# Kernel optimization log

Hardware: AMD Instinct MI355X
Metric: run time of the kernel (lower is better)

## Reference

```python
import jax, jax.numpy as jnp
import numpy as np

N, E = 20000, 320000
IN_F, EF, H, C = 2, 1, 128, 2
BN_S = 1.0 / float(np.sqrt(1.0 + 1e-5))  # eval-mode BatchNorm1d with running mean 0, var 1


def _gated_gcn_conv(h, e, src, dst, p, act, residual):
    # DGL GatedGCNConv: e' = C e + D h_src + E h_dst;
    # h' = A h + sum_{in-edges} sigmoid(e') * B h_src / (sum sigmoid(e') + 1e-6)
    Aw, Ab, Bw, Bb, Cw, Cb, Dw, Db, Ew, Eb, bhg, bhb, beg, beb = p
    h_in, e_in = h, e
    Ah = h @ Aw + Ab
    Bh = h @ Bw + Bb
    Dh = h @ Dw + Db
    Eh = h @ Ew + Eb
    e2 = e @ Cw + Cb + Dh[src] + Eh[dst]          # [E, H]
    sig = jax.nn.sigmoid(e2)
    num = jax.ops.segment_sum(sig * Bh[src], dst, num_segments=N)  # [N, H]
    den = jax.ops.segment_sum(sig, dst, num_segments=N)            # [N, H]
    h2 = Ah + num / (den + 1e-6)
    # BatchNorm (eval): (x - 0)/sqrt(1 + eps) * gamma + beta
    h2 = bhg * (h2 * BN_S) + bhb
    e2 = beg * (e2 * BN_S) + beb
    h2, e2 = act(h2), act(e2)
    if residual:
        h2 = h2 + h_in
        e2 = e2 + e_in
    return h2, e2


def _forward(node_feats, edge_feats, src, dst, P):
    (a0_w, a0_b, b0_w, b0_b, c0_w, c0_b, d0_w, d0_b, e0_w, e0_b,
     bnh0_g, bnh0_b, bne0_g, bne0_b,
     aL_w, aL_b, bL_w, bL_b, cL_w, cL_b, dL_w, dL_b, eL_w, eL_b,
     bnhL_g, bnhL_b, bneL_g, bneL_b,
     mlp_w1, mlp_b1, mlp_w2, mlp_b2) = P
    h, e = node_feats, edge_feats
    # layer 0: elu inside conv, residual off (2->128, 1->128)
    p0 = (a0_w, a0_b, b0_w, b0_b, c0_w, c0_b, d0_w, d0_b, e0_w, e0_b,
          bnh0_g, bnh0_b, bne0_g, bne0_b)
    h, e = _gated_gcn_conv(h, e, src, dst, p0, jax.nn.elu, residual=False)
    h = jax.nn.leaky_relu(h)
    e = jax.nn.leaky_relu(e)
    # layers 1..2: leaky_relu inside conv, residual on (128->128)
    for l in range(2):
        pl = (aL_w[l], aL_b[l], bL_w[l], bL_b[l], cL_w[l], cL_b[l],
              dL_w[l], dL_b[l], eL_w[l], eL_b[l],
              bnhL_g[l], bnhL_b[l], bneL_g[l], bneL_b[l])
        h, e = _gated_gcn_conv(h, e, src, dst, pl, jax.nn.leaky_relu, residual=True)
        h = jax.nn.leaky_relu(h)
        e = jax.nn.leaky_relu(e)
    # edge classifier: gather endpoints, concat with edge feats, MLP
    edge_repr = jnp.concatenate([h[src], h[dst], e], axis=1)  # [E, 3H]
    hid = jax.nn.relu(edge_repr @ mlp_w1 + mlp_b1)
    return hid @ mlp_w2 + mlp_b2                               # [E, C]


PARAM_NAMES = ["a0_w", "a0_b", "b0_w", "b0_b", "c0_w", "c0_b", "d0_w", "d0_b",
               "e0_w", "e0_b", "bnh0_g", "bnh0_b", "bne0_g", "bne0_b",
               "aL_w", "aL_b", "bL_w", "bL_b", "cL_w", "cL_b", "dL_w", "dL_b",
               "eL_w", "eL_b", "bnhL_g", "bnhL_b", "bneL_g", "bneL_b",
               "mlp_w1", "mlp_b1", "mlp_w2", "mlp_b2"]


def setup_inputs() -> dict:
    key = jax.random.key(0)
    ks = iter(jax.random.split(key, 64))
    nrm = lambda shp: jax.random.normal(next(ks), shp, dtype=jnp.float32) * 0.05
    inp = {}
    inp["node_feats"] = jax.random.normal(next(ks), (N, IN_F), dtype=jnp.float32)
    inp["edge_feats"] = jax.random.normal(next(ks), (E, EF), dtype=jnp.float32)
    inp["src"] = jax.random.randint(next(ks), (E,), 0, N, dtype=jnp.int32)
    inp["dst"] = jax.random.randint(next(ks), (E,), 0, N, dtype=jnp.int32)
    # layer 0 linears (A,B,D,E: in->H; C: edge->H), biases zero-init like common practice
    for nm, din in [("a0", IN_F), ("b0", IN_F), ("c0", EF), ("d0", IN_F), ("e0", IN_F)]:
        inp[nm + "_w"] = nrm((din, H))
        inp[nm + "_b"] = nrm((H,))
    inp["bnh0_g"] = jnp.ones((H,), jnp.float32)
    inp["bnh0_b"] = jnp.zeros((H,), jnp.float32)
    inp["bne0_g"] = jnp.ones((H,), jnp.float32)
    inp["bne0_b"] = jnp.zeros((H,), jnp.float32)
    # layers 1..2 stacked
    for nm in ["aL", "bL", "cL", "dL", "eL"]:
        inp[nm + "_w"] = nrm((2, H, H))
        inp[nm + "_b"] = nrm((2, H))
    inp["bnhL_g"] = jnp.ones((2, H), jnp.float32)
    inp["bnhL_b"] = jnp.zeros((2, H), jnp.float32)
    inp["bneL_g"] = jnp.ones((2, H), jnp.float32)
    inp["bneL_b"] = jnp.zeros((2, H), jnp.float32)
    # edge MLP
    inp["mlp_w1"] = nrm((3 * H, H))
    inp["mlp_b1"] = nrm((H,))
    inp["mlp_w2"] = nrm((H, C))
    inp["mlp_b2"] = nrm((C,))
    return inp


def reference(node_feats, edge_feats, src, dst,
              a0_w, a0_b, b0_w, b0_b, c0_w, c0_b, d0_w, d0_b, e0_w, e0_b,
              bnh0_g, bnh0_b, bne0_g, bne0_b,
              aL_w, aL_b, bL_w, bL_b, cL_w, cL_b, dL_w, dL_b, eL_w, eL_b,
              bnhL_g, bnhL_b, bneL_g, bneL_b,
              mlp_w1, mlp_b1, mlp_w2, mlp_b2):
    P = (a0_w, a0_b, b0_w, b0_b, c0_w, c0_b, d0_w, d0_b, e0_w, e0_b,
         bnh0_g, bnh0_b, bne0_g, bne0_b,
         aL_w, aL_b, bL_w, bL_b, cL_w, cL_b, dL_w, dL_b, eL_w, eL_b,
         bnhL_g, bnhL_b, bneL_g, bneL_b,
         mlp_w1, mlp_b1, mlp_w2, mlp_b2)
    return _forward(node_feats, edge_feats, src, dst, P)
```

## Files before the change

### kernel.cpp

```cpp
#include <hip/hip_runtime.h>
#include <hip/hip_bf16.h>
#include <math.h>

#define NN 20000
#define NE 320000
#define H 128
#define NH (NN * H)

typedef short bf16x8 __attribute__((ext_vector_type(8)));
typedef float f32x4 __attribute__((ext_vector_type(4)));
typedef unsigned short u16x8 __attribute__((ext_vector_type(8)));

__device__ __forceinline__ float lrelu(float x) { return x > 0.f ? x : 0.01f * x; }
__device__ __forceinline__ float eluf(float x)  { return x > 0.f ? x : expm1f(x); }
__device__ __forceinline__ float sigf(float x)  { return 1.f / (1.f + __expf(-x)); }
__device__ __forceinline__ unsigned short f2b(float x) {
    __hip_bfloat16 h = __float2bfloat16(x);
    return *reinterpret_cast<unsigned short*>(&h);
}
__device__ __forceinline__ float b2f(unsigned short u) {
    __hip_bfloat16 h = *reinterpret_cast<__hip_bfloat16*>(&u);
    return __bfloat162float(h);
}
#define BN_S 0.99999500003749973f

struct PackPtrs { const float* w[13]; };
__global__ __launch_bounds__(256) void k_pack(PackPtrs p, unsigned short* __restrict__ dst) {
    int gid = blockIdx.x * 256 + threadIdx.x;
    int m = gid >> 11;
    int r = gid & 2047;
    int t = r >> 8, kk = (r >> 6) & 3, lane = r & 63;
    const float* W = p.w[m];
    int col = t * 16 + (lane & 15);
    int krow = kk * 32 + (lane >> 4) * 8;
    unsigned short* o = dst + (size_t)m * 16384 + (size_t)r * 8;
#pragma unroll
    for (int j = 0; j < 8; ++j) o[j] = f2b(W[(krow + j) * H + col]);
}

__global__ __launch_bounds__(256) void k_deg(const int* __restrict__ dst, int* __restrict__ deg) {
    int e = blockIdx.x * 256 + threadIdx.x;
    if (e < NE) atomicAdd(&deg[dst[e]], 1);
}

__global__ __launch_bounds__(256) void k_scan(const int* __restrict__ deg,
                                              int* __restrict__ off, int* __restrict__ cursor) {
    __shared__ int sums[256];
    const int t = threadIdx.x;
    const int per = (NN + 255) / 256;
    const int base = t * per;
    int s = 0;
    for (int i = 0; i < per; ++i) { int idx = base + i; if (idx < NN) s += deg[idx]; }
    sums[t] = s;
    __syncthreads();
    for (int d = 1; d < 256; d <<= 1) {
        int v = (t >= d) ? sums[t - d] : 0;
        __syncthreads();
        sums[t] += v;
        __syncthreads();
    }
    int run = (t == 0) ? 0 : sums[t - 1];
    for (int i = 0; i < per; ++i) {
        int idx = base + i;
        if (idx < NN) { off[idx] = run; cursor[idx] = run; run += deg[idx]; }
    }
}

__global__ __launch_bounds__(256) void k_fill(const int* __restrict__ dst,
                                              int* __restrict__ cursor, int* __restrict__ csr) {
    int e = blockIdx.x * 256 + threadIdx.x;
    if (e < NE) {
        int pos = atomicAdd(&cursor[dst[e]], 1);
        csr[pos] = e;
    }
}

__global__ __launch_bounds__(256) void k_seqs(const int* __restrict__ csr,
                                              const int* __restrict__ src,
                                              const int* __restrict__ dst,
                                              int* __restrict__ srcseq,
                                              int* __restrict__ dstseq) {
    int pos = blockIdx.x * 256 + threadIdx.x;
    if (pos < NE) {
        int eid = csr[pos];
        srcseq[pos] = src[eid];
        dstseq[pos] = dst[eid];
    }
}

__global__ __launch_bounds__(256) void k_nodelin0(
        const float* __restrict__ nf,
        const float* __restrict__ wa, const float* __restrict__ ba,
        const float* __restrict__ wb, const float* __restrict__ bb,
        const float* __restrict__ wd, const float* __restrict__ bd,
        const float* __restrict__ we, const float* __restrict__ be,
        float* __restrict__ lin) {
    int idx = blockIdx.x * 256 + threadIdx.x;
    int n = idx >> 7, c = idx & 127;
    float x0 = nf[n * 2], x1 = nf[n * 2 + 1];
    lin[0 * NH + idx] = fmaf(x0, wa[c], fmaf(x1, wa[128 + c], ba[c]));
    lin[1 * NH + idx] = fmaf(x0, wb[c], fmaf(x1, wb[128 + c], bb[c]));
    lin[2 * NH + idx] = fmaf(x0, wd[c], fmaf(x1, wd[128 + c], bd[c]));
    lin[3 * NH + idx] = fmaf(x0, we[c], fmaf(x1, we[128 + c], be[c]));
}

__global__ __launch_bounds__(256) void k_edge0(
        const float* __restrict__ ef,
        const float* __restrict__ cw, const float* __restrict__ cb,
        const int* __restrict__ src, const int* __restrict__ dst,
        const float* __restrict__ lin,
        const float* __restrict__ g, const float* __restrict__ bt,
        unsigned short* __restrict__ ebuf) {
    const int tid = threadIdx.x;
    const int e  = blockIdx.x * 8 + (tid >> 5);
    const int c0 = (tid & 31) * 4;
    const int s = src[e], d = dst[e];
    const float ev = ef[e];
    const float4 cw4 = *(const float4*)(cw + c0);
    const float4 cb4 = *(const float4*)(cb + c0);
    const float4 Dh  = *(const float4*)(lin + 2 * NH + (size_t)s * H + c0);
    const float4 Eh  = *(const float4*)(lin + 3 * NH + (size_t)d * H + c0);
    const float4 g4  = *(const float4*)(g + c0);
    const float4 bt4 = *(const float4*)(bt + c0);
    float e2[4] = { fmaf(ev, cw4.x, cb4.x) + Dh.x + Eh.x,
                    fmaf(ev, cw4.y, cb4.y) + Dh.y + Eh.y,
                    fmaf(ev, cw4.z, cb4.z) + Dh.z + Eh.z,
                    fmaf(ev, cw4.w, cb4.w) + Dh.w + Eh.w };
    const float gg[4] = { g4.x, g4.y, g4.z, g4.w };
    const float bb[4] = { bt4.x, bt4.y, bt4.z, bt4.w };
    ushort4 u;
    u.x = f2b(lrelu(eluf(fmaf(gg[0], e2[0] * BN_S, bb[0]))));
    u.y = f2b(lrelu(eluf(fmaf(gg[1], e2[1] * BN_S, bb[1]))));
    u.z = f2b(lrelu(eluf(fmaf(gg[2], e2[2] * BN_S, bb[2]))));
    u.w = f2b(lrelu(eluf(fmaf(gg[3], e2[3] * BN_S, bb[3]))));
    *(ushort4*)(ebuf + (size_t)e * H + c0) = u;
}

__global__ __launch_bounds__(256) void k_agg0(
        const int* __restrict__ off, const int* __restrict__ deg,
        const int* __restrict__ csr, const int* __restrict__ srcseq,
        const float* __restrict__ ef, const float* __restrict__ cw, const float* __restrict__ cb,
        const float* __restrict__ lin,
        const float* __restrict__ g, const float* __restrict__ bt,
        float* __restrict__ hout) {
    const int tid = threadIdx.x;
    const int n = blockIdx.x * 2 + (tid >> 7);
    const int c = tid & 127;
    const int base = off[n], dg = deg[n];
    float num = 0.f, den = 0.f;
    const float Ehn = lin[3 * NH + (size_t)n * H + c];
    const float cwc = cw[c], cbc = cb[c];
    int i = 0;
    for (; i + 2 <= dg; i += 2) {
        int ea = csr[base + i], eb = csr[base + i + 1];
        int sa = srcseq[base + i], sb = srcseq[base + i + 1];
        float xa = fmaf(ef[ea], cwc, cbc) + lin[2 * NH + (size_t)sa * H + c] + Ehn;
        float xb = fmaf(ef[eb], cwc, cbc) + lin[2 * NH + (size_t)sb * H + c] + Ehn;
        float ga = sigf(xa), gb = sigf(xb);
        num = fmaf(ga, lin[1 * NH + (size_t)sa * H + c], num); den += ga;
        num = fmaf(gb, lin[1 * NH + (size_t)sb * H + c], num); den += gb;
    }
    if (i < dg) {
        int ea = csr[base + i];
        int sa = srcseq[base + i];
        float xa = fmaf(ef[ea], cwc, cbc) + lin[2 * NH + (size_t)sa * H + c] + Ehn;
        float ga = sigf(xa);
        num = fmaf(ga, lin[1 * NH + (size_t)sa * H + c], num); den += ga;
    }
    float h2 = lin[(size_t)n * H + c] + num / (den + 1e-6f);
    h2 = fmaf(g[c], h2 * BN_S, bt[c]);
    h2 = eluf(h2);
    hout[(size_t)n * H + c] = lrelu(h2);
}

__global__ __launch_bounds__(256) void k_agg(
        const int* __restrict__ off, const int* __restrict__ deg,
        const int* __restrict__ srcseq,
        const unsigned short* __restrict__ e2seq,
        const float* __restrict__ lin,
        const float* __restrict__ g, const float* __restrict__ bt,
        const float* __restrict__ hin, float* __restrict__ hout) {
    const int tid = threadIdx.x;
    const int n = blockIdx.x * 2 + (tid >> 7);
    const int c = tid & 127;
    const int base = off[n], dg = deg[n];
    float num = 0.f, den = 0.f;
    int i = 0;
    for (; i + 2 <= dg; i += 2) {
        int sa = srcseq[base + i], sb = srcseq[base + i + 1];
        float xa = b2f(e2seq[(size_t)(base + i) * H + c]);
        float xb = b2f(e2seq[(size_t)(base + i + 1) * H + c]);
        float ga = sigf(xa), gb = sigf(xb);
        num = fmaf(ga, lin[1 * NH + (size_t)sa * H + c], num); den += ga;
        num = fmaf(gb, lin[1 * NH + (size_t)sb * H + c], num); den += gb;
    }
    if (i < dg) {
        int sa = srcseq[base + i];
        float xa = b2f(e2seq[(size_t)(base + i) * H + c]);
        float ga = sigf(xa);
        num = fmaf(ga, lin[1 * NH + (size_t)sa * H + c], num); den += ga;
    }
    float h2 = lin[(size_t)n * H + c] + num / (den + 1e-6f);
    h2 = fmaf(g[c], h2 * BN_S, bt[c]);
    h2 = lrelu(h2);
    h2 += hin[(size_t)n * H + c];
    hout[(size_t)n * H + c] = lrelu(h2);
}

__global__ __launch_bounds__(256) void k_nodegemm(
        const float* __restrict__ h,
        const unsigned short* __restrict__ wpack,
        const float* __restrict__ ba, const float* __restrict__ bb,
        const float* __restrict__ bd, const float* __restrict__ be,
        float* __restrict__ lin) {
    __shared__ __align__(16) unsigned short AT[64][136];
    const int tid = threadIdx.x;
    const int nbase = blockIdx.x * 64;
    const int which = blockIdx.y;
    const unsigned short* Wp = wpack + (size_t)which * 16384;
    const float* B = which == 0 ? ba : which == 1 ? bb : which == 2 ? bd : be;
#pragma unroll
    for (int rep = 0; rep < 8; ++rep) {
        int flat = (rep * 256 + tid) * 4;
        int r = flat >> 7, k0 = flat & 127;
        int n = nbase + r;
        float4 v = make_float4(0.f, 0.f, 0.f, 0.f);
        if (n < NN) v = *(const float4*)(h + (size_t)n * H + k0);
        ushort4 u = { f2b(v.x), f2b(v.y), f2b(v.z), f2b(v.w) };
        *(ushort4*)(&AT[r][k0]) = u;
    }
    __syncthreads();
    const int lane = tid & 63, wave = tid >> 6;
    const int lrow = lane & 15, quad = lane >> 4;
    f32x4 acc[8] = {};
#pragma unroll
    for (int kk = 0; kk < 4; ++kk) {
        bf16x8 af = *(const bf16x8*)(&AT[wave * 16 + lrow][kk * 32 + quad * 8]);
#pragma unroll
        for (int t = 0; t < 8; ++t) {
            bf16x8 bfv = *(const bf16x8*)(Wp + ((t * 4 + kk) * 64 + lane) * 8);
            acc[t] = __builtin_amdgcn_mfma_f32_16x16x32_bf16(af, bfv, acc[t], 0, 0, 0);
        }
    }
#pragma unroll
    for (int t = 0; t < 8; ++t) {
        int col = t * 16 + lrow;
        float bv = B[col];
#pragma unroll
        for (int reg = 0; reg < 4; ++reg) {
            int n = nbase + wave * 16 + quad * 4 + reg;
            if (n < NN)
                lin[(size_t)which * NH + (size_t)n * H + col] = acc[t][reg] + bv;
        }
    }
}

__global__ __launch_bounds__(256) void k_edgegemm(
        unsigned short* __restrict__ ebuf,
        unsigned short* __restrict__ e2seq,
        const unsigned short* __restrict__ Wp,
        const float* __restrict__ cb,
        const int* __restrict__ csr,
        const int* __restrict__ srcseq, const int* __restrict__ dstseq,
        const float* __restrict__ lin,
        const float* __restrict__ g, const float* __restrict__ bt) {
    __shared__ __align__(16) unsigned short AT[64][136];
    const int tid = threadIdx.x;
    const int ebase = blockIdx.x * 64;
#pragma unroll
    for (int rep = 0; rep < 4; ++rep) {
        int flat = (rep * 256 + tid) * 8;
        int r = flat >> 7, k0 = flat & 127;
        int eid = csr[ebase + r];
        *(u16x8*)(&AT[r][k0]) = *(const u16x8*)(ebuf + (size_t)eid * H + k0);
    }
    __syncthreads();
    const int lane = tid & 63, wave = tid >> 6;
    const int lrow = lane & 15, quad = lane >> 4;
    f32x4 acc[8] = {};
#pragma unroll
    for (int kk = 0; kk < 4; ++kk) {
        bf16x8 af = *(const bf16x8*)(&AT[wave * 16 + lrow][kk * 32 + quad * 8]);
#pragma unroll
        for (int t = 0; t < 8; ++t) {
            bf16x8 bfv = *(const bf16x8*)(Wp + ((t * 4 + kk) * 64 + lane) * 8);
            acc[t] = __builtin_amdgcn_mfma_f32_16x16x32_bf16(af, bfv, acc[t], 0, 0, 0);
        }
    }
    const int r0 = ebase + wave * 16 + quad * 4;
    const int rr0 = wave * 16 + quad * 4;
    int eid[4], sv[4], dv[4];
#pragma unroll
    for (int reg = 0; reg < 4; ++reg) {
        eid[reg] = csr[r0 + reg];
        sv[reg]  = srcseq[r0 + reg];
        dv[reg]  = dstseq[r0 + reg];
    }
#pragma unroll
    for (int t = 0; t < 8; ++t) {
        int col = t * 16 + lrow;
        float cbv = cb[col], gv = g[col], btv = bt[col];
#pragma unroll
        for (int reg = 0; reg < 4; ++reg) {
            float Dh = lin[2 * NH + (size_t)sv[reg] * H + col];
            float Eh = lin[3 * NH + (size_t)dv[reg] * H + col];
            float e2 = acc[t][reg] + cbv + Dh + Eh;
            e2seq[(size_t)(r0 + reg) * H + col] = f2b(e2);
            float tt = lrelu(fmaf(gv, e2 * BN_S, btv));
            float ein = b2f(AT[rr0 + reg][col]);
            ebuf[(size_t)eid[reg] * H + col] = f2b(lrelu(tt + ein));
        }
    }
}

__global__ __launch_bounds__(256) void k_mlp(
        const float* __restrict__ h, const unsigned short* __restrict__ ebuf,
        const int* __restrict__ src, const int* __restrict__ dst,
        const unsigned short* __restrict__ w1p,
        const float* __restrict__ b1,
        const float* __restrict__ w2, const float* __restrict__ b2,
        float* __restrict__ out) {
    __shared__ __align__(16) unsigned short AT[64][136];
    const int tid = threadIdx.x;
    const int ebase = blockIdx.x * 64;
    const int lane = tid & 63, wave = tid >> 6;
    const int lrow = lane & 15, quad = lane >> 4;
    f32x4 acc[8] = {};
    for (int chunk = 0; chunk < 3; ++chunk) {
        if (chunk < 2) {
            const int* idx = chunk == 0 ? src : dst;
#pragma unroll
            for (int rep = 0; rep < 8; ++rep) {
                int flat = (rep * 256 + tid) * 4;
                int r = flat >> 7, k0 = flat & 127;
                int e = ebase + r;
                float4 v = *(const float4*)(h + (size_t)idx[e] * H + k0);
                ushort4 u = { f2b(v.x), f2b(v.y), f2b(v.z), f2b(v.w) };
                *(ushort4*)(&AT[r][k0]) = u;
            }
        } else {
#pragma unroll
            for (int rep = 0; rep < 4; ++rep) {
                int flat = (rep * 256 + tid) * 8;
                int r = flat >> 7, k0 = flat & 127;
                int e = ebase + r;
                *(u16x8*)(&AT[r][k0]) = *(const u16x8*)(ebuf + (size_t)e * H + k0);
            }
        }
        __syncthreads();
        const unsigned short* Wp = w1p + (size_t)chunk * 16384;
#pragma unroll
        for (int kk = 0; kk < 4; ++kk) {
            bf16x8 af = *(const bf16x8*)(&AT[wave * 16 + lrow][kk * 32 + quad * 8]);
#pragma unroll
            for (int t = 0; t < 8; ++t) {
                bf16x8 bfv = *(const bf16x8*)(Wp + ((t * 4 + kk) * 64 + lane) * 8);
                acc[t] = __builtin_amdgcn_mfma_f32_16x16x32_bf16(af, bfv, acc[t], 0, 0, 0);
            }
        }
        __syncthreads();
    }
    const float b20 = b2[0], b21 = b2[1];
#pragma unroll
    for (int reg = 0; reg < 4; ++reg) {
        float p0 = 0.f, p1 = 0.f;
#pragma unroll
        for (int t = 0; t < 8; ++t) {
            int col = t * 16 + lrow;
            float hv = fmaxf(acc[t][reg] + b1[col], 0.f);
            p0 = fmaf(hv, w2[col * 2], p0);
            p1 = fmaf(hv, w2[col * 2 + 1], p1);
        }
#pragma unroll
        for (int off = 8; off; off >>= 1) {
            p0 += __shfl_xor(p0, off, 16);
            p1 += __shfl_xor(p1, off, 16);
        }
        if (lrow == 0) {
            int e = ebase + wave * 16 + quad * 4 + reg;
            out[e * 2]     = p0 + b20;
            out[e * 2 + 1] = p1 + b21;
        }
    }
}

extern "C" void kernel_launch(void* const* d_in, const int* in_sizes, int n_in,
                              void* d_out, int out_size, void* d_ws, size_t ws_size,
                              hipStream_t stream) {
    const float* nf  = (const float*)d_in[0];
    const float* ef  = (const float*)d_in[1];
    const int*   src = (const int*)d_in[2];
    const int*   dst = (const int*)d_in[3];
    const float *a0w = (const float*)d_in[4],  *a0b = (const float*)d_in[5];
    const float *b0w = (const float*)d_in[6],  *b0b = (const float*)d_in[7];
    const float *c0w = (const float*)d_in[8],  *c0b = (const float*)d_in[9];
    const float *d0w = (const float*)d_in[10], *d0b = (const float*)d_in[11];
    const float *e0w = (const float*)d_in[12], *e0b = (const float*)d_in[13];
    const float *bnh0g = (const float*)d_in[14], *bnh0b = (const float*)d_in[15];
    const float *bne0g = (const float*)d_in[16], *bne0b = (const float*)d_in[17];
    const float *aLw = (const float*)d_in[18], *aLb = (const float*)d_in[19];
    const float *bLw = (const float*)d_in[20], *bLb = (const float*)d_in[21];
    const float *cLw = (const float*)d_in[22], *cLb = (const float*)d_in[23];
    const float *dLw = (const float*)d_in[24], *dLb = (const float*)d_in[25];
    const float *eLw = (const float*)d_in[26], *eLb = (const float*)d_in[27];
    const float *bnhLg = (const float*)d_in[28], *bnhLb = (const float*)d_in[29];
    const float *bneLg = (const float*)d_in[30], *bneLb = (const float*)d_in[31];
    const float *w1 = (const float*)d_in[32], *b1 = (const float*)d_in[33];
    const float *w2 = (const float*)d_in[34], *b2 = (const float*)d_in[35];
    float* out = (float*)d_out;

    char* ws = (char*)d_ws;
    unsigned short* ebuf  = (unsigned short*)ws;
    unsigned short* e2seq = ebuf + (size_t)NE * H;
    float* lin = (float*)(e2seq + (size_t)NE * H);
    float* h0  = lin + 4ull * NH;
    float* h1  = h0 + NH;
    int* deg    = (int*)(h1 + NH);
    int* off    = deg + NN;
    int* cursor = off + NN;
    int* csr    = cursor + NN;
    int* srcseq = csr + NE;
    int* dstseq = srcseq + NE;
    unsigned short* wpack = (unsigned short*)(dstseq + NE);

    PackPtrs pp;
    const size_t HH = (size_t)H * H;
    for (int l = 0; l < 2; ++l) {
        pp.w[l * 5 + 0] = aLw + l * HH;
        pp.w[l * 5 + 1] = bLw + l * HH;
        pp.w[l * 5 + 2] = dLw + l * HH;
        pp.w[l * 5 + 3] = eLw + l * HH;
        pp.w[l * 5 + 4] = cLw + l * HH;
    }
    pp.w[10] = w1; pp.w[11] = w1 + HH; pp.w[12] = w1 + 2 * HH;
    k_pack<<<104, 256, 0, stream>>>(pp, wpack);

    hipMemsetAsync(deg, 0, NN * sizeof(int), stream);
    k_deg<<<(NE + 255) / 256, 256, 0, stream>>>(dst, deg);
    k_scan<<<1, 256, 0, stream>>>(deg, off, cursor);
    k_fill<<<(NE + 255) / 256, 256, 0, stream>>>(dst, cursor, csr);
    k_seqs<<<(NE + 255) / 256, 256, 0, stream>>>(csr, src, dst, srcseq, dstseq);

    k_nodelin0<<<NN * H / 256, 256, 0, stream>>>(nf, a0w, a0b, b0w, b0b, d0w, d0b, e0w, e0b, lin);
    k_edge0<<<NE / 8, 256, 0, stream>>>(ef, c0w, c0b, src, dst, lin, bne0g, bne0b, ebuf);
    k_agg0<<<NN / 2, 256, 0, stream>>>(off, deg, csr, srcseq, ef, c0w, c0b,
                                       lin, bnh0g, bnh0b, h0);

    for (int l = 0; l < 2; ++l) {
        const float* hin = (l == 0) ? h0 : h1;
        float* hout      = (l == 0) ? h1 : h0;
        k_nodegemm<<<dim3(313, 4), 256, 0, stream>>>(hin,
            wpack + (size_t)l * 5 * 16384,
            aLb + l * H, bLb + l * H, dLb + l * H, eLb + l * H, lin);
        k_edgegemm<<<NE / 64, 256, 0, stream>>>(ebuf, e2seq,
                                                wpack + (size_t)(l * 5 + 4) * 16384,
                                                cLb + l * H, csr, srcseq, dstseq, lin,
                                                bneLg + l * H, bneLb + l * H);
        k_agg<<<NN / 2, 256, 0, stream>>>(off, deg, srcseq, e2seq,
                                          lin, bnhLg + l * H, bnhLb + l * H,
                                          hin, hout);
    }

    k_mlp<<<NE / 64, 256, 0, stream>>>(h0, ebuf, src, dst, wpack + 10ull * 16384,
                                       b1, w2, b2, out);

    (void)in_sizes; (void)n_in; (void)out_size; (void)ws_size;
}
```

Measured before the change: 764.1 us.

## Precompute node-side MLP projections per node and keep bf16 node feature copies

```diff
diff --git a/kernel.cpp b/kernel.cpp
--- a/kernel.cpp
+++ b/kernel.cpp
@@ -142,7 +142,7 @@
         const float* __restrict__ ef, const float* __restrict__ cw, const float* __restrict__ cb,
         const float* __restrict__ lin,
         const float* __restrict__ g, const float* __restrict__ bt,
-        float* __restrict__ hout) {
+        float* __restrict__ hout, unsigned short* __restrict__ hbout) {
     const int tid = threadIdx.x;
     const int n = blockIdx.x * 2 + (tid >> 7);
     const int c = tid & 127;
@@ -151,16 +151,22 @@
     const float Ehn = lin[3 * NH + (size_t)n * H + c];
     const float cwc = cw[c], cbc = cb[c];
     int i = 0;
-    for (; i + 2 <= dg; i += 2) {
-        int ea = csr[base + i], eb = csr[base + i + 1];
-        int sa = srcseq[base + i], sb = srcseq[base + i + 1];
-        float xa = fmaf(ef[ea], cwc, cbc) + lin[2 * NH + (size_t)sa * H + c] + Ehn;
-        float xb = fmaf(ef[eb], cwc, cbc) + lin[2 * NH + (size_t)sb * H + c] + Ehn;
-        float ga = sigf(xa), gb = sigf(xb);
-        num = fmaf(ga, lin[1 * NH + (size_t)sa * H + c], num); den += ga;
-        num = fmaf(gb, lin[1 * NH + (size_t)sb * H + c], num); den += gb;
-    }
-    if (i < dg) {
+    for (; i + 4 <= dg; i += 4) {
+        int e0 = csr[base + i],     e1 = csr[base + i + 1];
+        int e2_ = csr[base + i + 2], e3 = csr[base + i + 3];
+        int s0 = srcseq[base + i],     s1 = srcseq[base + i + 1];
+        int s2 = srcseq[base + i + 2], s3 = srcseq[base + i + 3];
+        float x0 = fmaf(ef[e0], cwc, cbc) + lin[2 * NH + (size_t)s0 * H + c] + Ehn;
+        float x1 = fmaf(ef[e1], cwc, cbc) + lin[2 * NH + (size_t)s1 * H + c] + Ehn;
+        float x2 = fmaf(ef[e2_], cwc, cbc) + lin[2 * NH + (size_t)s2 * H + c] + Ehn;
+        float x3 = fmaf(ef[e3], cwc, cbc) + lin[2 * NH + (size_t)s3 * H + c] + Ehn;
+        float g0 = sigf(x0), g1 = sigf(x1), g2 = sigf(x2), g3 = sigf(x3);
+        num = fmaf(g0, lin[1 * NH + (size_t)s0 * H + c], num); den += g0;
+        num = fmaf(g1, lin[1 * NH + (size_t)s1 * H + c], num); den += g1;
+        num = fmaf(g2, lin[1 * NH + (size_t)s2 * H + c], num); den += g2;
+        num = fmaf(g3, lin[1 * NH + (size_t)s3 * H + c], num); den += g3;
+    }
+    for (; i < dg; ++i) {
         int ea = csr[base + i];
         int sa = srcseq[base + i];
         float xa = fmaf(ef[ea], cwc, cbc) + lin[2 * NH + (size_t)sa * H + c] + Ehn;
@@ -170,7 +176,9 @@
     float h2 = lin[(size_t)n * H + c] + num / (den + 1e-6f);
     h2 = fmaf(g[c], h2 * BN_S, bt[c]);
     h2 = eluf(h2);
-    hout[(size_t)n * H + c] = lrelu(h2);
+    float r = lrelu(h2);
+    hout[(size_t)n * H + c] = r;
+    hbout[(size_t)n * H + c] = f2b(r);
 }
 
 __global__ __launch_bounds__(256) void k_agg(
@@ -179,22 +187,28 @@
         const unsigned short* __restrict__ e2seq,
         const float* __restrict__ lin,
         const float* __restrict__ g, const float* __restrict__ bt,
-        const float* __restrict__ hin, float* __restrict__ hout) {
+        const float* __restrict__ hin, float* __restrict__ hout,
+        unsigned short* __restrict__ hbout) {
     const int tid = threadIdx.x;
     const int n = blockIdx.x * 2 + (tid >> 7);
     const int c = tid & 127;
     const int base = off[n], dg = deg[n];
     float num = 0.f, den = 0.f;
     int i = 0;
-    for (; i + 2 <= dg; i += 2) {
-        int sa = srcseq[base + i], sb = srcseq[base + i + 1];
-        float xa = b2f(e2seq[(size_t)(base + i) * H + c]);
-        float xb = b2f(e2seq[(size_t)(base + i + 1) * H + c]);
-        float ga = sigf(xa), gb = sigf(xb);
-        num = fmaf(ga, lin[1 * NH + (size_t)sa * H + c], num); den += ga;
-        num = fmaf(gb, lin[1 * NH + (size_t)sb * H + c], num); den += gb;
-    }
-    if (i < dg) {
+    for (; i + 4 <= dg; i += 4) {
+        int s0 = srcseq[base + i],     s1 = srcseq[base + i + 1];
+        int s2 = srcseq[base + i + 2], s3 = srcseq[base + i + 3];
+        float x0 = b2f(e2seq[(size_t)(base + i) * H + c]);
+        float x1 = b2f(e2seq[(size_t)(base + i + 1) * H + c]);
+        float x2 = b2f(e2seq[(size_t)(base + i + 2) * H + c]);
+        float x3 = b2f(e2seq[(size_t)(base + i + 3) * H + c]);
+        float g0 = sigf(x0), g1 = sigf(x1), g2 = sigf(x2), g3 = sigf(x3);
+        num = fmaf(g0, lin[1 * NH + (size_t)s0 * H + c], num); den += g0;
+        num = fmaf(g1, lin[1 * NH + (size_t)s1 * H + c], num); den += g1;
+        num = fmaf(g2, lin[1 * NH + (size_t)s2 * H + c], num); den += g2;
+        num = fmaf(g3, lin[1 * NH + (size_t)s3 * H + c], num); den += g3;
+    }
+    for (; i < dg; ++i) {
         int sa = srcseq[base + i];
         float xa = b2f(e2seq[(size_t)(base + i) * H + c]);
         float ga = sigf(xa);
@@ -204,11 +218,13 @@
     h2 = fmaf(g[c], h2 * BN_S, bt[c]);
     h2 = lrelu(h2);
     h2 += hin[(size_t)n * H + c];
-    hout[(size_t)n * H + c] = lrelu(h2);
+    float r = lrelu(h2);
+    hout[(size_t)n * H + c] = r;
+    hbout[(size_t)n * H + c] = f2b(r);
 }
 
 __global__ __launch_bounds__(256) void k_nodegemm(
-        const float* __restrict__ h,
+        const unsigned short* __restrict__ hb,
         const unsigned short* __restrict__ wpack,
         const float* __restrict__ ba, const float* __restrict__ bb,
         const float* __restrict__ bd, const float* __restrict__ be,
@@ -220,14 +236,13 @@
     const unsigned short* Wp = wpack + (size_t)which * 16384;
     const float* B = which == 0 ? ba : which == 1 ? bb : which == 2 ? bd : be;
 #pragma unroll
-    for (int rep = 0; rep < 8; ++rep) {
-        int flat = (rep * 256 + tid) * 4;
+    for (int rep = 0; rep < 4; ++rep) {
+        int flat = (rep * 256 + tid) * 8;
         int r = flat >> 7, k0 = flat & 127;
         int n = nbase + r;
-        float4 v = make_float4(0.f, 0.f, 0.f, 0.f);
-        if (n < NN) v = *(const float4*)(h + (size_t)n * H + k0);
-        ushort4 u = { f2b(v.x), f2b(v.y), f2b(v.z), f2b(v.w) };
-        *(ushort4*)(&AT[r][k0]) = u;
+        u16x8 v = {};
+        if (n < NN) v = *(const u16x8*)(hb + (size_t)n * H + k0);
+        *(u16x8*)(&AT[r][k0]) = v;
     }
     __syncthreads();
     const int lane = tid & 63, wave = tid >> 6;
@@ -251,6 +266,51 @@
             int n = nbase + wave * 16 + quad * 4 + reg;
             if (n < NN)
                 lin[(size_t)which * NH + (size_t)n * H + col] = acc[t][reg] + bv;
+        }
+    }
+}
+
+__global__ __launch_bounds__(256) void k_pgemm(
+        const unsigned short* __restrict__ hb,
+        const unsigned short* __restrict__ w1p,
+        const float* __restrict__ b1,
+        float* __restrict__ P) {
+    __shared__ __align__(16) unsigned short AT[64][136];
+    const int tid = threadIdx.x;
+    const int nbase = blockIdx.x * 64;
+    const int y = blockIdx.y;
+    const unsigned short* Wp = w1p + (size_t)y * 16384;
+#pragma unroll
+    for (int rep = 0; rep < 4; ++rep) {
+        int flat = (rep * 256 + tid) * 8;
+        int r = flat >> 7, k0 = flat & 127;
+        int n = nbase + r;
+        u16x8 v = {};
+        if (n < NN) v = *(const u16x8*)(hb + (size_t)n * H + k0);
+        *(u16x8*)(&AT[r][k0]) = v;
+    }
+    __syncthreads();
+    const int lane = tid & 63, wave = tid >> 6;
+    const int lrow = lane & 15, quad = lane >> 4;
+    f32x4 acc[8] = {};
+#pragma unroll
+    for (int kk = 0; kk < 4; ++kk) {
+        bf16x8 af = *(const bf16x8*)(&AT[wave * 16 + lrow][kk * 32 + quad * 8]);
+#pragma unroll
+        for (int t = 0; t < 8; ++t) {
+            bf16x8 bfv = *(const bf16x8*)(Wp + ((t * 4 + kk) * 64 + lane) * 8);
+            acc[t] = __builtin_amdgcn_mfma_f32_16x16x32_bf16(af, bfv, acc[t], 0, 0, 0);
+        }
+    }
+#pragma unroll
+    for (int t = 0; t < 8; ++t) {
+        int col = t * 16 + lrow;
+        float bv = (y == 0) ? b1[col] : 0.f;
+#pragma unroll
+        for (int reg = 0; reg < 4; ++reg) {
+            int n = nbase + wave * 16 + quad * 4 + reg;
+            if (n < NN)
+                P[(size_t)y * NH + (size_t)n * H + col] = acc[t][reg] + bv;
         }
     }
 }
@@ -313,61 +373,53 @@
     }
 }
 
-__global__ __launch_bounds__(256) void k_mlp(
-        const float* __restrict__ h, const unsigned short* __restrict__ ebuf,
+__global__ __launch_bounds__(256) void k_mlp2(
+        const unsigned short* __restrict__ ebuf,
+        const float* __restrict__ P,
         const int* __restrict__ src, const int* __restrict__ dst,
-        const unsigned short* __restrict__ w1p,
-        const float* __restrict__ b1,
+        const unsigned short* __restrict__ w1p2,
         const float* __restrict__ w2, const float* __restrict__ b2,
         float* __restrict__ out) {
     __shared__ __align__(16) unsigned short AT[64][136];
     const int tid = threadIdx.x;
     const int ebase = blockIdx.x * 64;
+#pragma unroll
+    for (int rep = 0; rep < 4; ++rep) {
+        int flat = (rep * 256 + tid) * 8;
+        int r = flat >> 7, k0 = flat & 127;
+        *(u16x8*)(&AT[r][k0]) = *(const u16x8*)(ebuf + (size_t)(ebase + r) * H + k0);
+    }
+    __syncthreads();
     const int lane = tid & 63, wave = tid >> 6;
     const int lrow = lane & 15, quad = lane >> 4;
     f32x4 acc[8] = {};
-    for (int chunk = 0; chunk < 3; ++chunk) {
-        if (chunk < 2) {
-            const int* idx = chunk == 0 ? src : dst;
-#pragma unroll
-            for (int rep = 0; rep < 8; ++rep) {
-                int flat = (rep * 256 + tid) * 4;
-                int r = flat >> 7, k0 = flat & 127;
-                int e = ebase + r;
-                float4 v = *(const float4*)(h + (size_t)idx[e] * H + k0);
-                ushort4 u = { f2b(v.x), f2b(v.y), f2b(v.z), f2b(v.w) };
-                *(ushort4*)(&AT[r][k0]) = u;
-            }
-        } else {
-#pragma unroll
-            for (int rep = 0; rep < 4; ++rep) {
-                int flat = (rep * 256 + tid) * 8;
-                int r = flat >> 7, k0 = flat & 127;
-                int e = ebase + r;
-                *(u16x8*)(&AT[r][k0]) = *(const u16x8*)(ebuf + (size_t)e * H + k0);
-            }
-        }
-        __syncthreads();
-        const unsigned short* Wp = w1p + (size_t)chunk * 16384;
-#pragma unroll
-        for (int kk = 0; kk < 4; ++kk) {
-            bf16x8 af = *(const bf16x8*)(&AT[wave * 16 + lrow][kk * 32 + quad * 8]);
-#pragma unroll
-            for (int t = 0; t < 8; ++t) {
-                bf16x8 bfv = *(const bf16x8*)(Wp + ((t * 4 + kk) * 64 + lane) * 8);
-                acc[t] = __builtin_amdgcn_mfma_f32_16x16x32_bf16(af, bfv, acc[t], 0, 0, 0);
-            }
-        }
-        __syncthreads();
-    }
+#pragma unroll
+    for (int kk = 0; kk < 4; ++kk) {
+        bf16x8 af = *(const bf16x8*)(&AT[wave * 16 + lrow][kk * 32 + quad * 8]);
+#pragma unroll
+        for (int t = 0; t < 8; ++t) {
+            bf16x8 bfv = *(const bf16x8*)(w1p2 + ((t * 4 + kk) * 64 + lane) * 8);
+            acc[t] = __builtin_amdgcn_mfma_f32_16x16x32_bf16(af, bfv, acc[t], 0, 0, 0);
+        }
+    }
+    const int e0 = ebase + wave * 16 + quad * 4;
     const float b20 = b2[0], b21 = b2[1];
 #pragma unroll
     for (int reg = 0; reg < 4; ++reg) {
-        float p0 = 0.f, p1 = 0.f;
+        const int e = e0 + reg;
+        const int s = src[e], d = dst[e];
+        float p1v[8], p2v[8];
 #pragma unroll
         for (int t = 0; t < 8; ++t) {
             int col = t * 16 + lrow;
-            float hv = fmaxf(acc[t][reg] + b1[col], 0.f);
+            p1v[t] = P[(size_t)s * H + col];
+            p2v[t] = P[(size_t)NH + (size_t)d * H + col];
+        }
+        float p0 = 0.f, p1 = 0.f;
+#pragma unroll
+        for (int t = 0; t < 8; ++t) {
+            int col = t * 16 + lrow;
+            float hv = fmaxf(acc[t][reg] + p1v[t] + p2v[t], 0.f);
             p0 = fmaf(hv, w2[col * 2], p0);
             p1 = fmaf(hv, w2[col * 2 + 1], p1);
         }
@@ -377,7 +429,6 @@
             p1 += __shfl_xor(p1, off, 16);
         }
         if (lrow == 0) {
-            int e = ebase + wave * 16 + quad * 4 + reg;
             out[e * 2]     = p0 + b20;
             out[e * 2 + 1] = p1 + b21;
         }
@@ -415,13 +466,16 @@
     float* lin = (float*)(e2seq + (size_t)NE * H);
     float* h0  = lin + 4ull * NH;
     float* h1  = h0 + NH;
-    int* deg    = (int*)(h1 + NH);
+    unsigned short* hb0 = (unsigned short*)(h1 + NH);
+    unsigned short* hb1 = hb0 + NH;
+    int* deg    = (int*)(hb1 + NH);
     int* off    = deg + NN;
     int* cursor = off + NN;
     int* csr    = cursor + NN;
     int* srcseq = csr + NE;
     int* dstseq = srcseq + NE;
     unsigned short* wpack = (unsigned short*)(dstseq + NE);
+    float* P = (float*)e2seq;
 
     PackPtrs pp;
     const size_t HH = (size_t)H * H;
@@ -444,12 +498,14 @@
     k_nodelin0<<<NN * H / 256, 256, 0, stream>>>(nf, a0w, a0b, b0w, b0b, d0w, d0b, e0w, e0b, lin);
     k_edge0<<<NE / 8, 256, 0, stream>>>(ef, c0w, c0b, src, dst, lin, bne0g, bne0b, ebuf);
     k_agg0<<<NN / 2, 256, 0, stream>>>(off, deg, csr, srcseq, ef, c0w, c0b,
-                                       lin, bnh0g, bnh0b, h0);
+                                       lin, bnh0g, bnh0b, h0, hb0);
 
     for (int l = 0; l < 2; ++l) {
         const float* hin = (l == 0) ? h0 : h1;
         float* hout      = (l == 0) ? h1 : h0;
-        k_nodegemm<<<dim3(313, 4), 256, 0, stream>>>(hin,
+        const unsigned short* hbin = (l == 0) ? hb0 : hb1;
+        unsigned short* hbout      = (l == 0) ? hb1 : hb0;
+        k_nodegemm<<<dim3(313, 4), 256, 0, stream>>>(hbin,
             wpack + (size_t)l * 5 * 16384,
             aLb + l * H, bLb + l * H, dLb + l * H, eLb + l * H, lin);
         k_edgegemm<<<NE / 64, 256, 0, stream>>>(ebuf, e2seq,
@@ -458,11 +514,12 @@
                                                 bneLg + l * H, bneLb + l * H);
         k_agg<<<NN / 2, 256, 0, stream>>>(off, deg, srcseq, e2seq,
                                           lin, bnhLg + l * H, bnhLb + l * H,
-                                          hin, hout);
-    }
-
-    k_mlp<<<NE / 64, 256, 0, stream>>>(h0, ebuf, src, dst, wpack + 10ull * 16384,
-                                       b1, w2, b2, out);
+                                          hin, hout, hbout);
+    }
+
+    k_pgemm<<<dim3(313, 2), 256, 0, stream>>>(hb0, wpack + 10ull * 16384, b1, P);
+    k_mlp2<<<NE / 64, 256, 0, stream>>>(ebuf, P, src, dst, wpack + 12ull * 16384,
+                                        w2, b2, out);
 
     (void)in_sizes; (void)n_in; (void)out_size; (void)ws_size;
 }
```

Result: faster. 692.6 us (-9.4%).
